# Kernel optimization log

Measured on AMD Instinct MI355X. Metric: run time of the kernel, lower is better.

## Reference

```python
import jax, jax.numpy as jnp
import numpy as np

LN_EPS = 1e-5


def setup_inputs() -> dict:
    key = jax.random.key(0)
    ks = jax.random.split(key, 4)
    B, N, C, K = 512, 100, 256, 3
    query = jax.random.normal(ks[0], (B, N, C), dtype=jnp.float32)
    value = jax.random.normal(ks[1], (B, N, C), dtype=jnp.float32)
    # nn.Linear(C, N+K): weight stored as [out,in] in torch; here use [in,out]
    W_wl = jax.random.normal(ks[2], (C, N + K), dtype=jnp.float32) / np.sqrt(C)
    b_wl = jax.random.normal(ks[3], (N + K,), dtype=jnp.float32) * 0.01
    ln_gamma = jnp.ones((C,), dtype=jnp.float32)
    ln_beta = jnp.zeros((C,), dtype=jnp.float32)
    return {"query": query, "value": value, "W_wl": W_wl, "b_wl": b_wl,
            "ln_gamma": ln_gamma, "ln_beta": ln_beta}


def reference(query, value, W_wl, b_wl, ln_gamma, ln_beta):
    B, N, C = query.shape
    K = W_wl.shape[1] - N
    # dynamic conv weights from query: [B, N, K] depthwise + [B, N, N] pointwise
    dy = jnp.einsum('bnc,ck->bnk', query, W_wl) + b_wl
    dw = dy[:, :, :K]          # depthwise kernels, one per (b, proposal)
    pw = dy[:, :, K:]          # pointwise mixing matrix [B, N, N]
    # depthwise conv1d along C with 'same' padding (cross-correlation like torch)
    pad_l = (K - 1) // 2
    pad_r = K - 1 - pad_l
    vp = jnp.pad(value, ((0, 0), (0, 0), (pad_l, pad_r)))
    depth = jnp.zeros_like(value)
    for k in range(K):  # K is tiny (3): static unrolled loop
        depth = depth + dw[:, :, k:k + 1] * vp[:, :, k:k + C]
    depth = jax.nn.relu(depth)
    # pointwise conv (kernel size 1) == per-sample NxN mix over proposals
    out = jnp.einsum('bnm,bmc->bnc', pw, depth)
    # LayerNorm over C
    mu = jnp.mean(out, axis=-1, keepdims=True)
    var = jnp.var(out, axis=-1, keepdims=True)
    out = (out - mu) * jax.lax.rsqrt(var + LN_EPS) * ln_gamma + ln_beta
    return out
```

## Files before the change

### kernel.cpp

```cpp
#include <hip/hip_runtime.h>

#define NN 100
#define CC 256
#define NKK 103
#define LSA 72
#define LDPW 136
#define OTS 260

typedef __bf16 bf16;
typedef __bf16 bf16x4 __attribute__((ext_vector_type(4)));
typedef __bf16 bf16x8 __attribute__((ext_vector_type(8)));
typedef float f32x4 __attribute__((ext_vector_type(4)));

__global__ __launch_bounds__(512, 4)
void dysepconv_fused(const float* __restrict__ query,
                     const float* __restrict__ value,
                     const float* __restrict__ W,
                     const float* __restrict__ bwl,
                     const float* __restrict__ gamma,
                     const float* __restrict__ beta,
                     float* __restrict__ out)
{
    __shared__ __align__(16) bf16 PW[NN * LDPW];
    __shared__ __align__(16) bf16 R[100 * LSA + NKK * LSA];
    __shared__ float DW[NN][3];
    __shared__ float RP[8][NN][2];
    __shared__ float RS[NN][2];

    bf16*  Abuf = R;
    bf16*  Wbuf = R + 100 * LSA;
    float* OT   = (float*)R;

    const int t    = threadIdx.x;
    const int w    = t >> 6;
    const int lane = t & 63;
    const int ln16 = lane & 15;
    const int g    = lane >> 4;
    const int hi8  = g * 8;
    const int b    = blockIdx.x;

    const float* qb = query + (size_t)b * NN * CC;
    const float* vb = value + (size_t)b * NN * CC;

    f32x4 acc1[7];
    #pragma unroll
    for (int I = 0; I < 7; ++I) acc1[I] = (f32x4){0.f, 0.f, 0.f, 0.f};

    for (int kc = 0; kc < 4; ++kc) {
        const int k0 = kc * 64;
        __syncthreads();
        {
            f32x4 qv[4];
            #pragma unroll
            for (int p = 0; p < 4; ++p) {
                int idx = p * 512 + t;
                if (idx < 1600) {
                    int r = idx >> 4, j = (idx & 15) << 2;
                    qv[p] = *(const f32x4*)(qb + r * CC + k0 + j);
                }
            }
            #pragma unroll
            for (int p = 0; p < 4; ++p) {
                int idx = p * 512 + t;
                if (idx < 1600) {
                    int r = idx >> 4, j = (idx & 15) << 2;
                    bf16x4 s;
                    #pragma unroll
                    for (int i = 0; i < 4; ++i) s[i] = (bf16)qv[p][i];
                    *(bf16x4*)&Abuf[r * LSA + j] = s;
                }
            }
        }
        {
            float wv[13];
            #pragma unroll
            for (int p = 0; p < 13; ++p) {
                int idx = p * 512 + t;
                if (idx < 64 * NKK) {
                    int kk = idx / NKK, ka = idx - kk * NKK;
                    wv[p] = W[(size_t)(k0 + kk) * NKK + ka];
                }
            }
            #pragma unroll
            for (int p = 0; p < 13; ++p) {
                int idx = p * 512 + t;
                if (idx < 64 * NKK) {
                    int kk = idx / NKK, ka = idx - kk * NKK;
                    Wbuf[ka * LSA + kk] = (bf16)wv[p];
                }
            }
        }
        __syncthreads();

        if (w < 7) {
            const int rB = (w * 16 + ln16 < NKK) ? (w * 16 + ln16) : (NKK - 1);
            #pragma unroll
            for (int s = 0; s < 2; ++s) {
                bf16x8 bv = *(const bf16x8*)&Wbuf[rB * LSA + s * 32 + hi8];
                #pragma unroll
                for (int I = 0; I < 7; ++I) {
                    int row = I * 16 + ln16;
                    row = (row < NN) ? row : (NN - 1);
                    bf16x8 av = *(const bf16x8*)&Abuf[row * LSA + s * 32 + hi8];
                    acc1[I] = __builtin_amdgcn_mfma_f32_16x16x32_bf16(av, bv, acc1[I], 0, 0, 0);
                }
            }
        }
    }
    __syncthreads();

    for (int i = t; i < NN * 28; i += 512) {
        int r = i / 28, m = 100 + (i - (i / 28) * 28);
        PW[r * LDPW + m] = (bf16)0.f;
    }
    if (w < 7) {
        const int kap = w * 16 + ln16;
        const float bw = (kap < NKK) ? bwl[kap] : 0.f;
        #pragma unroll
        for (int I = 0; I < 7; ++I) {
            #pragma unroll
            for (int r = 0; r < 4; ++r) {
                int n = I * 16 + g * 4 + r;
                if (n < NN && kap < NKK) {
                    float v = acc1[I][r] + bw;
                    if (kap < 3) DW[n][kap] = v;
                    else         PW[n * LDPW + (kap - 3)] = (bf16)v;
                }
            }
        }
    }
    __syncthreads();

    f32x4 acc2[2][7];
    #pragma unroll
    for (int st = 0; st < 2; ++st)
        #pragma unroll
        for (int I = 0; I < 7; ++I) acc2[st][I] = (f32x4){0.f, 0.f, 0.f, 0.f};

    const int cb = w * 16 + ln16;
    #pragma unroll
    for (int ks = 0; ks < 4; ++ks) {
        float xv[8], yv[8];
        #pragma unroll
        for (int j = 0; j < 8; ++j) {
            int m = ks * 32 + hi8 + j;
            bool mv = (m < NN);
            const float* vr = vb + m * CC;
            xv[j] = mv ? vr[cb]       : 0.f;
            yv[j] = mv ? vr[cb + 128] : 0.f;
        }
        bf16x8 dv0, dv1;
        #pragma unroll
        for (int j = 0; j < 8; ++j) {
            int  m  = ks * 32 + hi8 + j;
            bool mv = (m < NN);
            int  mc = mv ? m : (NN - 1);
            float w0 = DW[mc][0], w1 = DW[mc][1], w2 = DW[mc][2];
            float x0 = xv[j], y0 = yv[j];
            float xm = __shfl(x0, (lane - 1) & 63), xp = __shfl(x0, (lane + 1) & 63);
            float ym = __shfl(y0, (lane - 1) & 63), yp = __shfl(y0, (lane + 1) & 63);
            if (ln16 == 0) {
                xm = (mv && cb > 0) ? vb[m * CC + cb - 1] : 0.f;
                ym = mv ? vb[m * CC + cb + 127] : 0.f;
            }
            if (ln16 == 15) {
                xp = mv ? vb[m * CC + cb + 1] : 0.f;
                yp = (mv && cb + 129 < CC) ? vb[m * CC + cb + 129] : 0.f;
            }
            float d0 = w0 * xm + w1 * x0 + w2 * xp;
            float d1 = w0 * ym + w1 * y0 + w2 * yp;
            dv0[j] = (bf16)(mv ? fmaxf(d0, 0.f) : 0.f);
            dv1[j] = (bf16)(mv ? fmaxf(d1, 0.f) : 0.f);
        }
        #pragma unroll
        for (int I = 0; I < 7; ++I) {
            int row = I * 16 + ln16;
            row = (row < NN) ? row : (NN - 1);
            bf16x8 af = *(const bf16x8*)&PW[row * LDPW + ks * 32 + hi8];
            acc2[0][I] = __builtin_amdgcn_mfma_f32_16x16x32_bf16(af, dv0, acc2[0][I], 0, 0, 0);
            acc2[1][I] = __builtin_amdgcn_mfma_f32_16x16x32_bf16(af, dv1, acc2[1][I], 0, 0, 0);
        }
    }

    #pragma unroll
    for (int I = 0; I < 7; ++I) {
        #pragma unroll
        for (int r = 0; r < 4; ++r) {
            float a = acc2[0][I][r], e = acc2[1][I][r];
            float s1 = a + e, s2 = a * a + e * e;
            #pragma unroll
            for (int mk = 1; mk < 16; mk <<= 1) {
                s1 += __shfl_xor(s1, mk);
                s2 += __shfl_xor(s2, mk);
            }
            int n = I * 16 + g * 4 + r;
            if (ln16 == 0 && n < NN) {
                RP[w][n][0] = s1;
                RP[w][n][1] = s2;
            }
        }
    }
    __syncthreads();
    if (t < NN) {
        float S1 = 0.f, S2 = 0.f;
        #pragma unroll
        for (int wi = 0; wi < 8; ++wi) { S1 += RP[wi][t][0]; S2 += RP[wi][t][1]; }
        float mu  = S1 * (1.f / 256.f);
        float var = S2 * (1.f / 256.f) - mu * mu;
        RS[t][0] = mu;
        RS[t][1] = rsqrtf(fmaxf(var, 0.f) + 1e-5f);
    }
    __syncthreads();

    const float gm0 = gamma[cb], gm1 = gamma[cb + 128];
    const float bt0 = beta[cb],  bt1 = beta[cb + 128];
    float* ob = out + (size_t)b * NN * CC;
    #pragma unroll
    for (int I = 0; I < 7; ++I) {
        #pragma unroll
        for (int r = 0; r < 4; ++r) {
            int n = I * 16 + g * 4 + r;
            if (n < NN) {
                float mu = RS[n][0], rs = RS[n][1];
                int rt = g * 4 + r;
                OT[rt * OTS + cb]       = (acc2[0][I][r] - mu) * rs * gm0 + bt0;
                OT[rt * OTS + cb + 128] = (acc2[1][I][r] - mu) * rs * gm1 + bt1;
            }
        }
        __syncthreads();
        #pragma unroll
        for (int p = 0; p < 2; ++p) {
            int idx  = p * 512 + t;
            int row  = idx >> 6, c4 = (idx & 63) << 2;
            int grow = I * 16 + row;
            if (grow < NN)
                *(f32x4*)(ob + grow * CC + c4) = *(const f32x4*)&OT[row * OTS + c4];
        }
        __syncthreads();
    }
}

extern "C" void kernel_launch(void* const* d_in, const int* in_sizes, int n_in,
                              void* d_out, int out_size, void* d_ws, size_t ws_size,
                              hipStream_t stream) {
    const float* query = (const float*)d_in[0];
    const float* value = (const float*)d_in[1];
    const float* W     = (const float*)d_in[2];
    const float* bwl   = (const float*)d_in[3];
    const float* gamma = (const float*)d_in[4];
    const float* beta  = (const float*)d_in[5];
    dysepconv_fused<<<dim3(512), dim3(512), 0, stream>>>(query, value, W, bwl, gamma, beta, (float*)d_out);
}
```

Before: 191.1 us.

## Split fused kernel into GEMM1 kernel and conv+GEMM2+LayerNorm kernel via workspace

The single fused kernel is split in two. The first computes the dynamic depthwise and pointwise weights and writes them to a global workspace. The second reloads them, then runs the depthwise conv, the pointwise MFMA GEMM and LayerNorm. The split lowers per-kernel register and LDS pressure, and the ks loop unroll is removed, which may raise occupancy. In exchange it adds a second launch and a global round trip for the weights.

```diff
diff --git a/kernel.cpp b/kernel.cpp
--- a/kernel.cpp
+++ b/kernel.cpp
@@ -6,6 +6,7 @@
 #define LSA 72
 #define LDPW 136
 #define OTS 260
+#define PWLD 112
 
 typedef __bf16 bf16;
 typedef __bf16 bf16x4 __attribute__((ext_vector_type(4)));
@@ -13,23 +14,13 @@
 typedef float f32x4 __attribute__((ext_vector_type(4)));
 
 __global__ __launch_bounds__(512, 4)
-void dysepconv_fused(const float* __restrict__ query,
-                     const float* __restrict__ value,
-                     const float* __restrict__ W,
-                     const float* __restrict__ bwl,
-                     const float* __restrict__ gamma,
-                     const float* __restrict__ beta,
-                     float* __restrict__ out)
+void k1_gemm1(const float* __restrict__ query, const float* __restrict__ W,
+              const float* __restrict__ bwl,
+              bf16* __restrict__ ws_pw, float* __restrict__ ws_dw)
 {
-    __shared__ __align__(16) bf16 PW[NN * LDPW];
     __shared__ __align__(16) bf16 R[100 * LSA + NKK * LSA];
-    __shared__ float DW[NN][3];
-    __shared__ float RP[8][NN][2];
-    __shared__ float RS[NN][2];
-
-    bf16*  Abuf = R;
-    bf16*  Wbuf = R + 100 * LSA;
-    float* OT   = (float*)R;
+    bf16* Abuf = R;
+    bf16* Wbuf = R + 100 * LSA;
 
     const int t    = threadIdx.x;
     const int w    = t >> 6;
@@ -38,9 +29,7 @@
     const int g    = lane >> 4;
     const int hi8  = g * 8;
     const int b    = blockIdx.x;
-
     const float* qb = query + (size_t)b * NN * CC;
-    const float* vb = value + (size_t)b * NN * CC;
 
     f32x4 acc1[7];
     #pragma unroll
@@ -109,10 +98,8 @@
     }
     __syncthreads();
 
-    for (int i = t; i < NN * 28; i += 512) {
-        int r = i / 28, m = 100 + (i - (i / 28) * 28);
-        PW[r * LDPW + m] = (bf16)0.f;
-    }
+    bf16*  PWs = R;
+    float* DWs = (float*)((char*)R + NN * PWLD * 2);
     if (w < 7) {
         const int kap = w * 16 + ln16;
         const float bw = (kap < NKK) ? bwl[kap] : 0.f;
@@ -123,11 +110,50 @@
                 int n = I * 16 + g * 4 + r;
                 if (n < NN && kap < NKK) {
                     float v = acc1[I][r] + bw;
-                    if (kap < 3) DW[n][kap] = v;
-                    else         PW[n * LDPW + (kap - 3)] = (bf16)v;
-                }
-            }
-        }
+                    if (kap < 3) DWs[n * 3 + kap] = v;
+                    else         PWs[n * PWLD + (kap - 3)] = (bf16)v;
+                }
+            }
+        }
+    }
+    __syncthreads();
+    bf16* gpw = ws_pw + (size_t)b * NN * PWLD;
+    for (int u = t; u < 1400; u += 512)
+        *(bf16x8*)(gpw + u * 8) = *(const bf16x8*)&PWs[u * 8];
+    if (t < 300) ws_dw[b * 300 + t] = DWs[t];
+}
+
+__global__ __launch_bounds__(512, 4)
+void k2_conv_gemm2_ln(const float* __restrict__ value,
+                      const bf16* __restrict__ ws_pw, const float* __restrict__ ws_dw,
+                      const float* __restrict__ gamma, const float* __restrict__ beta,
+                      float* __restrict__ out)
+{
+    __shared__ __align__(16) bf16 PW[NN * LDPW];
+    __shared__ float DW[NN][3];
+    __shared__ float RP[8][NN][2];
+    __shared__ float RS[NN][2];
+    __shared__ __align__(16) float OT[16 * OTS];
+
+    const int t    = threadIdx.x;
+    const int w    = t >> 6;
+    const int lane = t & 63;
+    const int ln16 = lane & 15;
+    const int g    = lane >> 4;
+    const int hi8  = g * 8;
+    const int b    = blockIdx.x;
+    const float* vb = value + (size_t)b * NN * CC;
+
+    const bf16* gpw = ws_pw + (size_t)b * NN * PWLD;
+    for (int u = t; u < 1300; u += 512) {
+        int row = u / 13, cu = u - (u / 13) * 13;
+        *(bf16x8*)&PW[row * LDPW + cu * 8] = *(const bf16x8*)(gpw + row * PWLD + cu * 8);
+    }
+    if (t < 300) DW[t / 3][t % 3] = ws_dw[b * 300 + t];
+    __syncthreads();
+    for (int i = t; i < NN * 28; i += 512) {
+        int r = i / 28, c = 100 + (i - (i / 28) * 28);
+        PW[r * LDPW + c] = (bf16)0.f;
     }
     __syncthreads();
 
@@ -138,7 +164,6 @@
         for (int I = 0; I < 7; ++I) acc2[st][I] = (f32x4){0.f, 0.f, 0.f, 0.f};
 
     const int cb = w * 16 + ln16;
-    #pragma unroll
     for (int ks = 0; ks < 4; ++ks) {
         float xv[8], yv[8];
         #pragma unroll
@@ -249,5 +274,10 @@
     const float* bwl   = (const float*)d_in[3];
     const float* gamma = (const float*)d_in[4];
     const float* beta  = (const float*)d_in[5];
-    dysepconv_fused<<<dim3(512), dim3(512), 0, stream>>>(query, value, W, bwl, gamma, beta, (float*)d_out);
+
+    bf16*  ws_pw = (bf16*)d_ws;
+    float* ws_dw = (float*)((char*)d_ws + (size_t)512 * NN * PWLD * 2);
+
+    k1_gemm1<<<dim3(512), dim3(512), 0, stream>>>(query, W, bwl, ws_pw, ws_dw);
+    k2_conv_gemm2_ln<<<dim3(512), dim3(512), 0, stream>>>(value, ws_pw, ws_dw, gamma, beta, (float*)d_out);
 }
```

After: 223.7 us. 17.0% more time.
